# Kernel tuning notes

Measured on AMD Instinct MI355X. Metric: run time of the kernel, lower is better.

Reference implementation:

```python
import jax, jax.numpy as jnp
import numpy as np

N_NODES = 100000
N_EDGES = 1600000
D_FEAT = 512
HIDDEN = 64
N_CLASS = 16
DROP_P = 0.5


def setup_inputs() -> dict:
    key = jax.random.key(0)
    ks = jax.random.split(key, 6)
    x = jax.random.normal(ks[0], (N_NODES, D_FEAT), dtype=jnp.float32)
    edge_index = jax.random.randint(ks[1], (2, N_EDGES), 0, N_NODES, dtype=jnp.int32)
    e_w = jax.random.uniform(ks[2], (N_EDGES,), dtype=jnp.float32)
    # Glorot-ish init for the two GCN layer weights, zero bias (PyG default)
    W1 = jax.random.normal(ks[3], (D_FEAT, HIDDEN), dtype=jnp.float32) / np.sqrt(D_FEAT)
    b1 = jnp.zeros((HIDDEN,), dtype=jnp.float32)
    W2 = jax.random.normal(ks[4], (HIDDEN, N_CLASS), dtype=jnp.float32) / np.sqrt(HIDDEN)
    b2 = jnp.zeros((N_CLASS,), dtype=jnp.float32)
    return {"x": x, "edge_index": edge_index, "e_w": e_w,
            "W1": W1, "b1": b1, "W2": W2, "b2": b2}


def _gcn_conv(x, src, dst, w, W, b, num_nodes):
    """PyG GCNConv: linear transform, then symmetric-normalized scatter-add."""
    h = x @ W                                   # [N, out]
    deg = jax.ops.segment_sum(w, dst, num_segments=num_nodes)   # weighted in-degree
    dis = jnp.where(deg > 0, jax.lax.rsqrt(jnp.maximum(deg, 1e-12)), 0.0)
    norm = dis[src] * w * dis[dst]              # [E_total]
    msg = h[src] * norm[:, None]                # gather + scale  [E_total, out]
    out = jax.ops.segment_sum(msg, dst, num_segments=num_nodes)  # scatter-add
    return out + b


def reference(x, edge_index, e_w, W1, b1, W2, b2):
    n = x.shape[0]
    # add self-loops with weight 1 (GCNConv default)
    loops = jnp.arange(n, dtype=edge_index.dtype)
    src = jnp.concatenate([edge_index[0], loops])
    dst = jnp.concatenate([edge_index[1], loops])
    w = jnp.concatenate([e_w, jnp.ones((n,), dtype=e_w.dtype)])

    h = _gcn_conv(x, src, dst, w, W1, b1, n)
    h = jax.nn.relu(h)
    # F.dropout default p=0.5, training=True: deterministic fixed mask here
    keep = jax.random.bernoulli(jax.random.key(42), 1.0 - DROP_P, h.shape)
    h = jnp.where(keep, h / (1.0 - DROP_P), 0.0)

    x_out = _gcn_conv(h, src, dst, w, W2, b2, n)
    return jax.nn.log_softmax(x_out, axis=1), x_out
```

## Files before the change

kernel.cpp:

```cpp
#include <hip/hip_runtime.h>
#include <stdint.h>

#define N_NODES 100000
#define N_EDGES 1600000
#define D_FEAT  512
#define HIDDEN  64
#define N_CLASS 16
#define CAP     64
#define NBKT    196
#define BCAP    10240
#define EPB     4096
#define NWG1    ((N_EDGES + EPB - 1) / EPB)
#define GEMM1_BLKS ((N_NODES + 127) / 128)

typedef __bf16 bf16_t;
typedef bf16_t bf16x8 __attribute__((ext_vector_type(8)));
typedef float  f32x4  __attribute__((ext_vector_type(4)));

__device__ __forceinline__ unsigned rotl32(unsigned x, int d) {
    return (x << d) | (x >> (32 - d));
}
__device__ __forceinline__ void tf_round(unsigned& x0, unsigned& x1, int r) {
    x0 += x1; x1 = rotl32(x1, r); x1 ^= x0;
}
__device__ __forceinline__ uint2 threefry_0_42(unsigned c0, unsigned c1) {
    const unsigned ks0 = 0u, ks1 = 42u, ks2 = 0x1BD11BDAu ^ 0u ^ 42u;
    unsigned x0 = c0 + ks0, x1 = c1 + ks1;
    tf_round(x0,x1,13); tf_round(x0,x1,15); tf_round(x0,x1,26); tf_round(x0,x1,6);
    x0 += ks1; x1 += ks2 + 1u;
    tf_round(x0,x1,17); tf_round(x0,x1,29); tf_round(x0,x1,16); tf_round(x0,x1,24);
    x0 += ks2; x1 += ks0 + 2u;
    tf_round(x0,x1,13); tf_round(x0,x1,15); tf_round(x0,x1,26); tf_round(x0,x1,6);
    x0 += ks0; x1 += ks1 + 3u;
    tf_round(x0,x1,17); tf_round(x0,x1,29); tf_round(x0,x1,16); tf_round(x0,x1,24);
    x0 += ks1; x1 += ks2 + 4u;
    tf_round(x0,x1,13); tf_round(x0,x1,15); tf_round(x0,x1,26); tf_round(x0,x1,6);
    x0 += ks2; x1 += ks0 + 5u;
    return make_uint2(x0, x1);
}

__launch_bounds__(256)
__global__ void k_prep_bin(const float* __restrict__ W1, bf16_t* __restrict__ Wfg,
                           const int* __restrict__ src, const int* __restrict__ dst,
                           const float* __restrict__ w,
                           int* __restrict__ bucket_cursor, int2* __restrict__ bkt) {
    __shared__ int hist[NBKT];
    __shared__ int binbase[NBKT];
    int tid = threadIdx.x;
    int bid = blockIdx.x;
    if (bid < 128) {
        int e = bid * 256 + tid;
        int k = e >> 6, col = e & 63;
        int kstep = k >> 5, gg = (k >> 3) & 3, e8 = k & 7;
        int cf = col >> 4, lane = (col & 15) | (gg << 4);
        Wfg[(((kstep << 2) + cf) << 9) + (lane << 3) + e8] = (bf16_t)W1[e];
        return;
    }
    int b0 = bid - 128;
    int c4 = b0 * (EPB / 4);
    for (int t = tid; t < NBKT; t += 256) hist[t] = 0;
    __syncthreads();
    int rk[16]; int dd[16];
    #pragma unroll
    for (int i = 0; i < EPB / 1024; ++i) {
        int e4 = c4 + tid + 256 * i;
        if (e4 * 4 < N_EDGES) {
            int4 d = ((const int4*)dst)[e4];
            dd[4*i+0] = d.x; dd[4*i+1] = d.y; dd[4*i+2] = d.z; dd[4*i+3] = d.w;
            rk[4*i+0] = atomicAdd(&hist[d.x >> 9], 1);
            rk[4*i+1] = atomicAdd(&hist[d.y >> 9], 1);
            rk[4*i+2] = atomicAdd(&hist[d.z >> 9], 1);
            rk[4*i+3] = atomicAdd(&hist[d.w >> 9], 1);
        }
    }
    __syncthreads();
    for (int t = tid; t < NBKT; t += 256)
        binbase[t] = hist[t] ? atomicAdd(&bucket_cursor[t], hist[t]) : 0;
    __syncthreads();
    #pragma unroll
    for (int i = 0; i < EPB / 1024; ++i) {
        int e4 = c4 + tid + 256 * i;
        if (e4 * 4 < N_EDGES) {
            int4 s  = ((const int4*)src)[e4];
            int4 wv = ((const int4*)w)[e4];
            int ss[4] = {s.x, s.y, s.z, s.w};
            int ww[4] = {wv.x, wv.y, wv.z, wv.w};
            #pragma unroll
            for (int q = 0; q < 4; ++q) {
                int d = dd[4*i+q];
                int b = d >> 9;
                int pos = binbase[b] + rk[4*i+q];
                if (pos < BCAP)
                    bkt[(size_t)b * BCAP + pos] =
                        make_int2(ss[q] | ((d & 511) << 17), ww[q]);
            }
        }
    }
}

__launch_bounds__(256)
__global__ void k_build(const int* __restrict__ bucket_cursor, const int2* __restrict__ bkt,
                        int2* __restrict__ slots, int* __restrict__ cursor,
                        float* __restrict__ dis) {
    __shared__ int   cur[512];
    __shared__ float dg[512];
    int b = blockIdx.x, tid = threadIdx.x;
    cur[tid] = 0; cur[tid + 256] = 0;
    dg[tid] = 0.f; dg[tid + 256] = 0.f;
    __syncthreads();
    int cnt = bucket_cursor[b]; if (cnt > BCAP) cnt = BCAP;
    for (int e = tid; e < cnt; e += 256) {
        int2 p = bkt[(size_t)b * BCAP + e];
        int dl = ((unsigned)p.x) >> 17;
        int s  = p.x & 0x1FFFF;
        int rank = atomicAdd(&cur[dl], 1);
        if (rank < CAP)
            slots[((((size_t)b << 9) | dl) << 6) + rank] = make_int2(s, p.y);
        atomicAdd(&dg[dl], __int_as_float(p.y));
    }
    __syncthreads();
    #pragma unroll
    for (int t = 0; t < 2; ++t) {
        int loc = tid + 256 * t;
        int node = (b << 9) + loc;
        if (node < N_NODES) {
            cursor[node] = cur[loc];
            dis[node] = rsqrtf(dg[loc] + 1.0f);
        }
    }
}

__launch_bounds__(256)
__global__ void k_gemm1(const float* __restrict__ x, const bf16_t* __restrict__ Wfg,
                        const float* __restrict__ dis, bf16_t* __restrict__ h1) {
    __shared__ bf16_t Wf[16384];
    int tid = threadIdx.x;
    int w = tid >> 6, l = tid & 63;
    int r = l & 15, g = l >> 4;
    int wrow = blockIdx.x * 128 + w * 32;
    f32x4 acc[2][4] = {};
    const float* xp0 = x + (size_t)(wrow + r) * D_FEAT + 8 * g;
    const float* xp1 = x + (size_t)(wrow + 16 + r) * D_FEAT + 8 * g;
    bool ok0 = (wrow + r) < N_NODES;
    bool ok1 = (wrow + 16 + r) < N_NODES;

    #pragma unroll
    for (int h = 0; h < 2; ++h) {
        if (h) __syncthreads();
        {
            const int4* sW = (const int4*)(Wfg + h * 16384);
            int4* dW = (int4*)Wf;
            #pragma unroll
            for (int t = 0; t < 8; ++t) dW[tid + 256 * t] = sW[tid + 256 * t];
        }
        __syncthreads();
        #pragma unroll
        for (int t2 = 0; t2 < 8; ++t2) {
            int t = h * 8 + t2;
            float4 p0 = make_float4(0.f,0.f,0.f,0.f), q0 = p0, p1 = p0, q1 = p0;
            if (ok0) {
                p0 = *(const float4*)(xp0 + t * 32);
                q0 = *(const float4*)(xp0 + t * 32 + 4);
            }
            if (ok1) {
                p1 = *(const float4*)(xp1 + t * 32);
                q1 = *(const float4*)(xp1 + t * 32 + 4);
            }
            bf16x8 a0, a1;
            a0[0]=(bf16_t)p0.x; a0[1]=(bf16_t)p0.y; a0[2]=(bf16_t)p0.z; a0[3]=(bf16_t)p0.w;
            a0[4]=(bf16_t)q0.x; a0[5]=(bf16_t)q0.y; a0[6]=(bf16_t)q0.z; a0[7]=(bf16_t)q0.w;
            a1[0]=(bf16_t)p1.x; a1[1]=(bf16_t)p1.y; a1[2]=(bf16_t)p1.z; a1[3]=(bf16_t)p1.w;
            a1[4]=(bf16_t)q1.x; a1[5]=(bf16_t)q1.y; a1[6]=(bf16_t)q1.z; a1[7]=(bf16_t)q1.w;
            #pragma unroll
            for (int cf = 0; cf < 4; ++cf) {
                bf16x8 b = *(const bf16x8*)&Wf[(((t2 << 2) + cf) << 9) + (l << 3)];
                acc[0][cf] = __builtin_amdgcn_mfma_f32_16x16x32_bf16(a0, b, acc[0][cf], 0, 0, 0);
                acc[1][cf] = __builtin_amdgcn_mfma_f32_16x16x32_bf16(a1, b, acc[1][cf], 0, 0, 0);
            }
        }
    }
    #pragma unroll
    for (int rf = 0; rf < 2; ++rf)
        #pragma unroll
        for (int q = 0; q < 4; ++q) {
            int row = wrow + rf * 16 + 4 * g + q;
            if (row < N_NODES) {
                float dv = dis[row];
                #pragma unroll
                for (int cf = 0; cf < 4; ++cf)
                    h1[(size_t)row * HIDDEN + cf * 16 + r] = (bf16_t)(dv * acc[rf][cf][q]);
            }
        }
}

__launch_bounds__(256)
__global__ void k_agg1(const bf16_t* __restrict__ h1, const int2* __restrict__ slots,
                       const int* __restrict__ cursor, const float* __restrict__ dis,
                       const float* __restrict__ b1, const float* __restrict__ W2,
                       bf16_t* __restrict__ g) {
    __shared__ float W2s[HIDDEN * 17];
    __shared__ float h2s[4][HIDDEN];
    int tid = threadIdx.x;
    #pragma unroll
    for (int t = 0; t < 4; ++t) {
        int e = tid + 256 * t;
        W2s[(e >> 4) * 17 + (e & 15)] = W2[e];
    }
    int i = (blockIdx.x * blockDim.x + tid) >> 6;
    int l = tid & 63;
    int w = tid >> 6;
    int h = l >> 5, s32 = l & 31;
    float di = (i < N_NODES) ? dis[i] : 0.f;
    if (i < N_NODES) {
        int cnt = cursor[i]; cnt = cnt > CAP ? CAP : cnt;
        const int2* sl = &slots[(size_t)i << 6];
        float a0 = 0.f, a1 = 0.f;
        float c0 = 0.f, c1 = 0.f;
        if (h == 0) {
            unsigned v = *(const unsigned*)&h1[(size_t)i * HIDDEN + 2 * s32];
            a0 = __uint_as_float(v << 16);
            a1 = __uint_as_float(v & 0xffff0000u);
        }
        int p = h;
        for (; p + 14 < cnt; p += 16) {
            int2 e0 = sl[p],      e1 = sl[p + 2],  e2 = sl[p + 4],  e3 = sl[p + 6];
            int2 e4 = sl[p + 8],  e5 = sl[p + 10], e6 = sl[p + 12], e7 = sl[p + 14];
            float n0 = __int_as_float(e0.y), n1 = __int_as_float(e1.y);
            float n2 = __int_as_float(e2.y), n3 = __int_as_float(e3.y);
            float n4 = __int_as_float(e4.y), n5 = __int_as_float(e5.y);
            float n6 = __int_as_float(e6.y), n7 = __int_as_float(e7.y);
            unsigned v0 = *(const unsigned*)&h1[(size_t)e0.x * HIDDEN + 2 * s32];
            unsigned v1 = *(const unsigned*)&h1[(size_t)e1.x * HIDDEN + 2 * s32];
            unsigned v2 = *(const unsigned*)&h1[(size_t)e2.x * HIDDEN + 2 * s32];
            unsigned v3 = *(const unsigned*)&h1[(size_t)e3.x * HIDDEN + 2 * s32];
            unsigned v4 = *(const unsigned*)&h1[(size_t)e4.x * HIDDEN + 2 * s32];
            unsigned v5 = *(const unsigned*)&h1[(size_t)e5.x * HIDDEN + 2 * s32];
            unsigned v6 = *(const unsigned*)&h1[(size_t)e6.x * HIDDEN + 2 * s32];
            unsigned v7 = *(const unsigned*)&h1[(size_t)e7.x * HIDDEN + 2 * s32];
            a0 += n0 * __uint_as_float(v0 << 16);
            a1 += n0 * __uint_as_float(v0 & 0xffff0000u);
            c0 += n1 * __uint_as_float(v1 << 16);
            c1 += n1 * __uint_as_float(v1 & 0xffff0000u);
            a0 += n2 * __uint_as_float(v2 << 16);
            a1 += n2 * __uint_as_float(v2 & 0xffff0000u);
            c0 += n3 * __uint_as_float(v3 << 16);
            c1 += n3 * __uint_as_float(v3 & 0xffff0000u);
            a0 += n4 * __uint_as_float(v4 << 16);
            a1 += n4 * __uint_as_float(v4 & 0xffff0000u);
            c0 += n5 * __uint_as_float(v5 << 16);
            c1 += n5 * __uint_as_float(v5 & 0xffff0000u);
            a0 += n6 * __uint_as_float(v6 << 16);
            a1 += n6 * __uint_as_float(v6 & 0xffff0000u);
            c0 += n7 * __uint_as_float(v7 << 16);
            c1 += n7 * __uint_as_float(v7 & 0xffff0000u);
        }
        for (; p + 6 < cnt; p += 8) {
            int2 e0 = sl[p], e1 = sl[p + 2], e2 = sl[p + 4], e3 = sl[p + 6];
            float n0 = __int_as_float(e0.y), n1 = __int_as_float(e1.y);
            float n2 = __int_as_float(e2.y), n3 = __int_as_float(e3.y);
            unsigned v0 = *(const unsigned*)&h1[(size_t)e0.x * HIDDEN + 2 * s32];
            unsigned v1 = *(const unsigned*)&h1[(size_t)e1.x * HIDDEN + 2 * s32];
            unsigned v2 = *(const unsigned*)&h1[(size_t)e2.x * HIDDEN + 2 * s32];
            unsigned v3 = *(const unsigned*)&h1[(size_t)e3.x * HIDDEN + 2 * s32];
            a0 += n0 * __uint_as_float(v0 << 16);
            a1 += n0 * __uint_as_float(v0 & 0xffff0000u);
            c0 += n1 * __uint_as_float(v1 << 16);
            c1 += n1 * __uint_as_float(v1 & 0xffff0000u);
            a0 += n2 * __uint_as_float(v2 << 16);
            a1 += n2 * __uint_as_float(v2 & 0xffff0000u);
            c0 += n3 * __uint_as_float(v3 << 16);
            c1 += n3 * __uint_as_float(v3 & 0xffff0000u);
        }
        for (; p < cnt; p += 2) {
            int2 e0 = sl[p];
            float n = __int_as_float(e0.y);
            unsigned v = *(const unsigned*)&h1[(size_t)e0.x * HIDDEN + 2 * s32];
            a0 += n * __uint_as_float(v << 16);
            a1 += n * __uint_as_float(v & 0xffff0000u);
        }
        a0 += c0; a1 += c1;
        a0 += __shfl_xor(a0, 32);
        a1 += __shfl_xor(a1, 32);
        int f = 2 * s32 + h;
        float av = di * (h ? a1 : a0) + b1[f];
        av = fmaxf(av, 0.f);
        unsigned idx = (unsigned)i * HIDDEN + f;
        uint2 rr = threefry_0_42(0u, idx);
        h2s[w][f] = ((rr.x ^ rr.y) & 0x80000000u) ? 0.f : av * 2.f;
    } else {
        h2s[w][2 * s32 + h] = 0.f;
    }
    __syncthreads();
    int j = tid & 15, q = (tid >> 4) & 3;
    int node = blockIdx.x * 4 + w;
    float pk = 0.f;
    #pragma unroll
    for (int ff = 0; ff < 16; ++ff) {
        int fr = q * 16 + ff;
        pk += h2s[w][fr] * W2s[fr * 17 + j];
    }
    pk += __shfl_xor(pk, 16, 64);
    pk += __shfl_xor(pk, 32, 64);
    if (q == 0 && node < N_NODES) g[(size_t)node * N_CLASS + j] = (bf16_t)(di * pk);
}

__launch_bounds__(256)
__global__ void k_out(const bf16_t* __restrict__ g, const int2* __restrict__ slots,
                      const int* __restrict__ cursor, const float* __restrict__ dis,
                      const float* __restrict__ b2, float* __restrict__ out) {
    int i = (blockIdx.x * blockDim.x + threadIdx.x) >> 4;
    int j = threadIdx.x & 15;
    if (i >= N_NODES) return;
    float di = dis[i];
    float acc = (float)g[(size_t)i * N_CLASS + j];
    float acc2 = 0.f;
    int cnt = cursor[i]; cnt = cnt > CAP ? CAP : cnt;
    const int2* sl = &slots[(size_t)i << 6];
    int p = 0;
    for (; p + 8 <= cnt; p += 8) {
        int2 e0 = sl[p],     e1 = sl[p + 1], e2 = sl[p + 2], e3 = sl[p + 3];
        int2 e4 = sl[p + 4], e5 = sl[p + 5], e6 = sl[p + 6], e7 = sl[p + 7];
        float v0 = (float)g[(size_t)e0.x * N_CLASS + j];
        float v1 = (float)g[(size_t)e1.x * N_CLASS + j];
        float v2 = (float)g[(size_t)e2.x * N_CLASS + j];
        float v3 = (float)g[(size_t)e3.x * N_CLASS + j];
        float v4 = (float)g[(size_t)e4.x * N_CLASS + j];
        float v5 = (float)g[(size_t)e5.x * N_CLASS + j];
        float v6 = (float)g[(size_t)e6.x * N_CLASS + j];
        float v7 = (float)g[(size_t)e7.x * N_CLASS + j];
        acc  += __int_as_float(e0.y) * v0 + __int_as_float(e1.y) * v1
              + __int_as_float(e2.y) * v2 + __int_as_float(e3.y) * v3;
        acc2 += __int_as_float(e4.y) * v4 + __int_as_float(e5.y) * v5
              + __int_as_float(e6.y) * v6 + __int_as_float(e7.y) * v7;
    }
    for (; p + 4 <= cnt; p += 4) {
        int2 e0 = sl[p], e1 = sl[p + 1], e2 = sl[p + 2], e3 = sl[p + 3];
        float v0 = (float)g[(size_t)e0.x * N_CLASS + j];
        float v1 = (float)g[(size_t)e1.x * N_CLASS + j];
        float v2 = (float)g[(size_t)e2.x * N_CLASS + j];
        float v3 = (float)g[(size_t)e3.x * N_CLASS + j];
        acc  += __int_as_float(e0.y) * v0 + __int_as_float(e1.y) * v1;
        acc2 += __int_as_float(e2.y) * v2 + __int_as_float(e3.y) * v3;
    }
    for (; p < cnt; ++p) {
        int2 e0 = sl[p];
        acc += __int_as_float(e0.y) * (float)g[(size_t)e0.x * N_CLASS + j];
    }
    acc += acc2;
    acc = di * acc + b2[j];
    float xo = acc;
    float m = acc;
    #pragma unroll
    for (int d = 1; d < 16; d <<= 1) m = fmaxf(m, __shfl_xor(m, d, 16));
    float ex = expf(acc - m);
    float s = ex;
    #pragma unroll
    for (int d = 1; d < 16; d <<= 1) s += __shfl_xor(s, d, 16);
    float ls = (acc - m) - logf(s);
    out[(size_t)i * N_CLASS + j] = ls;
    out[(size_t)N_NODES * N_CLASS + (size_t)i * N_CLASS + j] = xo;
}

extern "C" void kernel_launch(void* const* d_in, const int* in_sizes, int n_in,
                              void* d_out, int out_size, void* d_ws, size_t ws_size,
                              hipStream_t stream) {
    const float* x  = (const float*)d_in[0];
    const int*   ei = (const int*)d_in[1];
    const float* ew = (const float*)d_in[2];
    const float* W1 = (const float*)d_in[3];
    const float* b1 = (const float*)d_in[4];
    const float* W2 = (const float*)d_in[5];
    const float* b2 = (const float*)d_in[6];
    float* out = (float*)d_out;
    const int* src = ei;
    const int* dst = ei + N_EDGES;

    size_t off = 0;
    char* wsb = (char*)d_ws;
    auto alloc = [&](size_t n) -> char* {
        char* p = wsb + off;
        off = (off + n + 255) & ~(size_t)255;
        return p;
    };
    int*    cursor = (int*)   alloc((size_t)N_NODES * 4);
    float*  dis    = (float*) alloc((size_t)N_NODES * 4);
    int*    bcur   = (int*)   alloc(NBKT * 4);
    bf16_t* Wfg    = (bf16_t*)alloc(32768 * 2);
    int2*   slots  = (int2*)  alloc((size_t)N_NODES * CAP * 8);
    bf16_t* h1     = (bf16_t*)alloc((size_t)N_NODES * HIDDEN * 2);
    int2*   bkt    = (int2*)  alloc((size_t)NBKT * BCAP * 8);
    bf16_t* g      = (bf16_t*)alloc((size_t)N_NODES * N_CLASS * 2);

    hipMemsetAsync(bcur, 0, NBKT * 4, stream);

    k_prep_bin<<<128 + NWG1, 256, 0, stream>>>(W1, Wfg, src, dst, ew, bcur, bkt);
    k_build   <<<NBKT, 256, 0, stream>>>(bcur, bkt, slots, cursor, dis);
    k_gemm1   <<<GEMM1_BLKS, 256, 0, stream>>>(x, Wfg, dis, h1);
    k_agg1    <<<(N_NODES + 3) / 4, 256, 0, stream>>>(h1, slots, cursor, dis, b1, W2, g);
    k_out     <<<(N_NODES * 16 + 255) / 256, 256, 0, stream>>>(g, slots, cursor, dis, b2, out);
}
```

Measured before the change: 186.2 us.

## Merge bucket build and first GEMM into one launch, defer source scaling

The CSR build and the layer-1 GEMM become one kernel: the first NBKT blocks build the slots and degrees, and the remaining blocks run the GEMM. This is possible because the GEMM no longer scales rows by dis. The source-side dis factor moves into the aggregation loop as an extra gathered load per edge. The aim is to remove a kernel boundary and let the bandwidth-heavy GEMM overlap with the atomic-heavy build, at the cost of an extra random dis gather per edge in k_agg1.

```diff
diff --git a/kernel.cpp b/kernel.cpp
--- a/kernel.cpp
+++ b/kernel.cpp
@@ -99,45 +99,50 @@
 }
 
 __launch_bounds__(256)
-__global__ void k_build(const int* __restrict__ bucket_cursor, const int2* __restrict__ bkt,
-                        int2* __restrict__ slots, int* __restrict__ cursor,
-                        float* __restrict__ dis) {
-    __shared__ int   cur[512];
-    __shared__ float dg[512];
-    int b = blockIdx.x, tid = threadIdx.x;
-    cur[tid] = 0; cur[tid + 256] = 0;
-    dg[tid] = 0.f; dg[tid + 256] = 0.f;
-    __syncthreads();
-    int cnt = bucket_cursor[b]; if (cnt > BCAP) cnt = BCAP;
-    for (int e = tid; e < cnt; e += 256) {
-        int2 p = bkt[(size_t)b * BCAP + e];
-        int dl = ((unsigned)p.x) >> 17;
-        int s  = p.x & 0x1FFFF;
-        int rank = atomicAdd(&cur[dl], 1);
-        if (rank < CAP)
-            slots[((((size_t)b << 9) | dl) << 6) + rank] = make_int2(s, p.y);
-        atomicAdd(&dg[dl], __int_as_float(p.y));
-    }
-    __syncthreads();
-    #pragma unroll
-    for (int t = 0; t < 2; ++t) {
-        int loc = tid + 256 * t;
-        int node = (b << 9) + loc;
-        if (node < N_NODES) {
-            cursor[node] = cur[loc];
-            dis[node] = rsqrtf(dg[loc] + 1.0f);
-        }
-    }
-}
-
-__launch_bounds__(256)
-__global__ void k_gemm1(const float* __restrict__ x, const bf16_t* __restrict__ Wfg,
-                        const float* __restrict__ dis, bf16_t* __restrict__ h1) {
-    __shared__ bf16_t Wf[16384];
+__global__ void k_build_gemm1(const int* __restrict__ bucket_cursor,
+                              const int2* __restrict__ bkt,
+                              int2* __restrict__ slots, int* __restrict__ cursor,
+                              float* __restrict__ dis,
+                              const float* __restrict__ x,
+                              const bf16_t* __restrict__ Wfg,
+                              bf16_t* __restrict__ h1) {
+    __shared__ __align__(16) char smem[32768];
     int tid = threadIdx.x;
+    int bid = blockIdx.x;
+    if (bid < NBKT) {
+        int* cur  = (int*)smem;
+        float* dg = (float*)(smem + 2048);
+        int b = bid;
+        cur[tid] = 0; cur[tid + 256] = 0;
+        dg[tid] = 0.f; dg[tid + 256] = 0.f;
+        __syncthreads();
+        int cnt = bucket_cursor[b]; if (cnt > BCAP) cnt = BCAP;
+        for (int e = tid; e < cnt; e += 256) {
+            int2 p = bkt[(size_t)b * BCAP + e];
+            int dl = ((unsigned)p.x) >> 17;
+            int s  = p.x & 0x1FFFF;
+            int rank = atomicAdd(&cur[dl], 1);
+            if (rank < CAP)
+                slots[((((size_t)b << 9) | dl) << 6) + rank] = make_int2(s, p.y);
+            atomicAdd(&dg[dl], __int_as_float(p.y));
+        }
+        __syncthreads();
+        #pragma unroll
+        for (int t = 0; t < 2; ++t) {
+            int loc = tid + 256 * t;
+            int node = (b << 9) + loc;
+            if (node < N_NODES) {
+                cursor[node] = cur[loc];
+                dis[node] = rsqrtf(dg[loc] + 1.0f);
+            }
+        }
+        return;
+    }
+    bf16_t* Wf = (bf16_t*)smem;
+    int gb = bid - NBKT;
     int w = tid >> 6, l = tid & 63;
     int r = l & 15, g = l >> 4;
-    int wrow = blockIdx.x * 128 + w * 32;
+    int wrow = gb * 128 + w * 32;
     f32x4 acc[2][4] = {};
     const float* xp0 = x + (size_t)(wrow + r) * D_FEAT + 8 * g;
     const float* xp1 = x + (size_t)(wrow + 16 + r) * D_FEAT + 8 * g;
@@ -182,15 +187,13 @@
     #pragma unroll
     for (int rf = 0; rf < 2; ++rf)
         #pragma unroll
-        for (int q = 0; q < 4; ++q) {
-            int row = wrow + rf * 16 + 4 * g + q;
-            if (row < N_NODES) {
-                float dv = dis[row];
-                #pragma unroll
-                for (int cf = 0; cf < 4; ++cf)
-                    h1[(size_t)row * HIDDEN + cf * 16 + r] = (bf16_t)(dv * acc[rf][cf][q]);
-            }
-        }
+        for (int cf = 0; cf < 4; ++cf)
+            #pragma unroll
+            for (int q = 0; q < 4; ++q) {
+                int row = wrow + rf * 16 + 4 * g + q;
+                int col = cf * 16 + r;
+                if (row < N_NODES) h1[(size_t)row * HIDDEN + col] = (bf16_t)acc[rf][cf][q];
+            }
 }
 
 __launch_bounds__(256)
@@ -218,17 +221,15 @@
         float c0 = 0.f, c1 = 0.f;
         if (h == 0) {
             unsigned v = *(const unsigned*)&h1[(size_t)i * HIDDEN + 2 * s32];
-            a0 = __uint_as_float(v << 16);
-            a1 = __uint_as_float(v & 0xffff0000u);
+            a0 = di * __uint_as_float(v << 16);
+            a1 = di * __uint_as_float(v & 0xffff0000u);
         }
         int p = h;
         for (; p + 14 < cnt; p += 16) {
             int2 e0 = sl[p],      e1 = sl[p + 2],  e2 = sl[p + 4],  e3 = sl[p + 6];
             int2 e4 = sl[p + 8],  e5 = sl[p + 10], e6 = sl[p + 12], e7 = sl[p + 14];
-            float n0 = __int_as_float(e0.y), n1 = __int_as_float(e1.y);
-            float n2 = __int_as_float(e2.y), n3 = __int_as_float(e3.y);
-            float n4 = __int_as_float(e4.y), n5 = __int_as_float(e5.y);
-            float n6 = __int_as_float(e6.y), n7 = __int_as_float(e7.y);
+            float d0 = dis[e0.x], d1 = dis[e1.x], d2 = dis[e2.x], d3 = dis[e3.x];
+            float d4 = dis[e4.x], d5 = dis[e5.x], d6 = dis[e6.x], d7 = dis[e7.x];
             unsigned v0 = *(const unsigned*)&h1[(size_t)e0.x * HIDDEN + 2 * s32];
             unsigned v1 = *(const unsigned*)&h1[(size_t)e1.x * HIDDEN + 2 * s32];
             unsigned v2 = *(const unsigned*)&h1[(size_t)e2.x * HIDDEN + 2 * s32];
@@ -237,6 +238,10 @@
             unsigned v5 = *(const unsigned*)&h1[(size_t)e5.x * HIDDEN + 2 * s32];
             unsigned v6 = *(const unsigned*)&h1[(size_t)e6.x * HIDDEN + 2 * s32];
             unsigned v7 = *(const unsigned*)&h1[(size_t)e7.x * HIDDEN + 2 * s32];
+            float n0 = d0 * __int_as_float(e0.y), n1 = d1 * __int_as_float(e1.y);
+            float n2 = d2 * __int_as_float(e2.y), n3 = d3 * __int_as_float(e3.y);
+            float n4 = d4 * __int_as_float(e4.y), n5 = d5 * __int_as_float(e5.y);
+            float n6 = d6 * __int_as_float(e6.y), n7 = d7 * __int_as_float(e7.y);
             a0 += n0 * __uint_as_float(v0 << 16);
             a1 += n0 * __uint_as_float(v0 & 0xffff0000u);
             c0 += n1 * __uint_as_float(v1 << 16);
@@ -256,12 +261,13 @@
         }
         for (; p + 6 < cnt; p += 8) {
             int2 e0 = sl[p], e1 = sl[p + 2], e2 = sl[p + 4], e3 = sl[p + 6];
-            float n0 = __int_as_float(e0.y), n1 = __int_as_float(e1.y);
-            float n2 = __int_as_float(e2.y), n3 = __int_as_float(e3.y);
+            float d0 = dis[e0.x], d1 = dis[e1.x], d2 = dis[e2.x], d3 = dis[e3.x];
             unsigned v0 = *(const unsigned*)&h1[(size_t)e0.x * HIDDEN + 2 * s32];
             unsigned v1 = *(const unsigned*)&h1[(size_t)e1.x * HIDDEN + 2 * s32];
             unsigned v2 = *(const unsigned*)&h1[(size_t)e2.x * HIDDEN + 2 * s32];
             unsigned v3 = *(const unsigned*)&h1[(size_t)e3.x * HIDDEN + 2 * s32];
+            float n0 = d0 * __int_as_float(e0.y), n1 = d1 * __int_as_float(e1.y);
+            float n2 = d2 * __int_as_float(e2.y), n3 = d3 * __int_as_float(e3.y);
             a0 += n0 * __uint_as_float(v0 << 16);
             a1 += n0 * __uint_as_float(v0 & 0xffff0000u);
             c0 += n1 * __uint_as_float(v1 << 16);
@@ -273,7 +279,7 @@
         }
         for (; p < cnt; p += 2) {
             int2 e0 = sl[p];
-            float n = __int_as_float(e0.y);
+            float n = dis[e0.x] * __int_as_float(e0.y);
             unsigned v = *(const unsigned*)&h1[(size_t)e0.x * HIDDEN + 2 * s32];
             a0 += n * __uint_as_float(v << 16);
             a1 += n * __uint_as_float(v & 0xffff0000u);
@@ -393,9 +399,9 @@
 
     hipMemsetAsync(bcur, 0, NBKT * 4, stream);
 
-    k_prep_bin<<<128 + NWG1, 256, 0, stream>>>(W1, Wfg, src, dst, ew, bcur, bkt);
-    k_build   <<<NBKT, 256, 0, stream>>>(bcur, bkt, slots, cursor, dis);
-    k_gemm1   <<<GEMM1_BLKS, 256, 0, stream>>>(x, Wfg, dis, h1);
-    k_agg1    <<<(N_NODES + 3) / 4, 256, 0, stream>>>(h1, slots, cursor, dis, b1, W2, g);
-    k_out     <<<(N_NODES * 16 + 255) / 256, 256, 0, stream>>>(g, slots, cursor, dis, b2, out);
-}
+    k_prep_bin   <<<128 + NWG1, 256, 0, stream>>>(W1, Wfg, src, dst, ew, bcur, bkt);
+    k_build_gemm1<<<NBKT + GEMM1_BLKS, 256, 0, stream>>>(bcur, bkt, slots, cursor, dis,
+                                                         x, Wfg, h1);
+    k_agg1       <<<(N_NODES + 3) / 4, 256, 0, stream>>>(h1, slots, cursor, dis, b1, W2, g);
+    k_out        <<<(N_NODES * 16 + 255) / 256, 256, 0, stream>>>(g, slots, cursor, dis, b2, out);
+}
```

After: 191.9 us. +3.1%, slower.
